# Optimization experiments

Measured on AMD Instinct MI355X. Metric: run time of the kernel, lower is better.

The kernel has to match this reference:

```python
import jax, jax.numpy as jnp
import numpy as np
import math

HEAD_DIM = 64
RP_DIM = 256
B, H, N = 4, 8, 4096
EPS = 1e-4  # performer positive-feature epsilon


def _ortho_gaussian_matrix(m, d, seed=0):
    # gaussian_orthogonal_random_matrix, scaling=0: stack QR-orthogonalized
    # d x d gaussian blocks, scale rows by norms of an iid gaussian matrix.
    rng = np.random.default_rng(seed)
    blocks = []
    for _ in range(int(np.ceil(m / d))):
        g = rng.standard_normal((d, d))
        q, _ = np.linalg.qr(g)
        blocks.append(q.T)
    mat = np.concatenate(blocks, axis=0)[:m]
    multiplier = np.linalg.norm(rng.standard_normal((m, d)), axis=1)
    return (multiplier[:, None] * mat).astype(np.float32)


def _softmax_features(x, proj, is_query):
    # FAVOR+ positive random features: ratio * exp(Wx - ||x||^2/2 - stab) + eps
    ratio = proj.shape[0] ** -0.5
    xp = jnp.einsum('bhnd,md->bhnm', x, proj)
    diag = 0.5 * jnp.sum(x * x, axis=-1, keepdims=True)
    if is_query:
        stab = jnp.max(xp, axis=-1, keepdims=True)
    else:
        stab = jnp.max(xp, axis=(-1, -2), keepdims=True)
    return ratio * (jnp.exp(xp - diag - stab) + EPS)


def setup_inputs() -> dict:
    key = jax.random.key(0)
    kq, kk, kv = jax.random.split(key, 3)
    Q = jax.random.normal(kq, (B, H, N, HEAD_DIM), dtype=jnp.float32)
    K = jax.random.normal(kk, (B, H, N, HEAD_DIM), dtype=jnp.float32)
    V = jax.random.normal(kv, (B, H, N, HEAD_DIM), dtype=jnp.float32)
    mask = jnp.ones((B, N), dtype=jnp.float32)
    projection = jnp.asarray(_ortho_gaussian_matrix(RP_DIM, HEAD_DIM, seed=0))
    return {'Q': Q, 'K': K, 'V': V, 'mask': mask, 'projection': projection}


def reference(Q, K, V, mask, projection):
    scale = HEAD_DIM ** -0.25  # 1/sqrt(sqrt(head_dim))
    m = mask[:, None, :, None]
    q = Q * scale
    k = K * scale * m
    v = V * m
    phi_q = _softmax_features(q, projection, is_query=True)   # [b,h,n,m]
    phi_k = _softmax_features(k, projection, is_query=False)  # [b,h,n,m]
    # non-causal linear attention
    k_sum = jnp.sum(phi_k, axis=2)                                   # [b,h,m]
    D_inv = 1.0 / jnp.einsum('bhnm,bhm->bhn', phi_q, k_sum)          # [b,h,n]
    context = jnp.einsum('bhnm,bhne->bhme', phi_k, v)                # [b,h,m,e]
    out = jnp.einsum('bhme,bhnm,bhn->bhne', context, phi_q, D_inv)   # [b,h,n,e]
    return out
```

## Files before the change

kernel.cpp:

```cpp
#include <hip/hip_runtime.h>
#include <hip/hip_bf16.h>


typedef __attribute__((ext_vector_type(8))) short short8;
typedef __attribute__((ext_vector_type(4))) float floatx4;

constexpr int BB = 4, HH = 8, NN = 4096, DD = 64, MM = 256, BH = 32;
constexpr int NCH = 16;
constexpr float SCALE = 0.3535533905932738f;
constexpr float RATIO = 0.0625f;
constexpr float EPSI  = 1e-4f;
constexpr float NEGINF = -3.4e38f;

__device__ inline unsigned pk2(float a, float b) {
  unsigned ua = __float_as_uint(a) + 0x8000u;
  unsigned ub = __float_as_uint(b) + 0x8000u;
  return (ua >> 16) | (ub & 0xffff0000u);
}
__device__ inline float hif(float x) {
  return __uint_as_float((__float_as_uint(x) + 0x8000u) & 0xffff0000u);
}
__device__ inline unsigned short bhi(float x) {
  return (unsigned short)((__float_as_uint(x) + 0x8000u) >> 16);
}
__device__ inline int ph16(int i) { return (i & 56) | ((i + (i >> 3)) & 7); }

union Frag { short8 s8; unsigned u[4]; };

__device__ inline void atomicMaxF(float* a, float v) {
  unsigned* ai = (unsigned*)a;
  unsigned old = __atomic_load_n(ai, __ATOMIC_RELAXED);
  while (__uint_as_float(old) < v) {
    unsigned assumed = old;
    old = atomicCAS(ai, assumed, __float_as_uint(v));
    if (old == assumed) break;
  }
}

__global__ __launch_bounds__(256) void prep_kernel(
    const float* __restrict__ proj, unsigned short* __restrict__ projH,
    unsigned short* __restrict__ projL, float* __restrict__ stabk,
    float* __restrict__ Vs, float* __restrict__ ctxsum,
    float* __restrict__ ksE) {
  const int i = blockIdx.x * 256 + threadIdx.x;
  float v = proj[i];
  projH[i] = bhi(v);
  projL[i] = bhi(v - hif(v));
  if (i < BH) stabk[i] = NEGINF;
  if (i < 2048) { Vs[i] = 0.f; ctxsum[i] = 0.f; }
  if (i < 8192) ksE[i] = 0.f;
}

template <bool PARTIAL>
__global__ __launch_bounds__(256) void kside_kernel(
    const float* __restrict__ K, const float* __restrict__ V,
    const float* __restrict__ mask,
    const unsigned short* __restrict__ projH, const unsigned short* __restrict__ projL,
    float* __restrict__ stabk, float* __restrict__ ksE,
    float* __restrict__ ctxOut, float* __restrict__ Vs) {
  const int bh = blockIdx.y, b = bh >> 3;
  const int t = threadIdx.x;
  const int w = t >> 6, l = t & 63, c = l & 15, sq = l >> 4;
  const int m0 = w * 64;

  __shared__ __align__(16) unsigned short sK[2][32 * 72];
  __shared__ __align__(16) unsigned short sVt[2][64 * 40];
  __shared__ float sDiag[32];
  __shared__ float sRed[4];
  __shared__ float sVsum[4][64];
  __shared__ __align__(16) unsigned short sPhi[4][2][512];

  Frag Bp[4][2][2];
#pragma unroll
  for (int tt = 0; tt < 4; ++tt)
#pragma unroll
    for (int s = 0; s < 2; ++s) {
      const size_t o = (size_t)(m0 + tt * 16 + c) * DD + s * 32 + sq * 8;
      Bp[tt][s][0].s8 = *(const short8*)&projH[o];
      Bp[tt][s][1].s8 = *(const short8*)&projL[o];
    }

  floatx4 ctxacc[4][4];
#pragma unroll
  for (int i = 0; i < 4; ++i)
#pragma unroll
    for (int j = 0; j < 4; ++j) ctxacc[i][j] = (floatx4){0.f, 0.f, 0.f, 0.f};
  float ksac[4] = {0.f, 0.f, 0.f, 0.f};
  float mxloc = NEGINF;
  float vsacc = 0.f;

  const int r0 = blockIdx.x * 256;

  for (int ch = 0; ch < 8; ++ch) {
    const int rb = r0 + ch * 32;
    __syncthreads();

#pragma unroll
    for (int rep = 0; rep < 2; ++rep) {
      const int f = t + rep * 256;
      const int n = f >> 4, dg = f & 15;
      const float mk = mask[b * NN + rb + n];
      const float msc = mk * SCALE;
      float4 kv = *(const float4*)(K + ((size_t)bh * NN + rb + n) * DD + dg * 4);
      float k0 = kv.x * msc, k1 = kv.y * msc, k2 = kv.z * msc, k3 = kv.w * msc;
      float ss = fmaf(k0, k0, fmaf(k1, k1, fmaf(k2, k2, k3 * k3)));
      ss += __shfl_xor(ss, 1); ss += __shfl_xor(ss, 2);
      ss += __shfl_xor(ss, 4); ss += __shfl_xor(ss, 8);
      if (dg == 0) sDiag[n] = 0.5f * ss;
      unsigned h0 = pk2(k0, k1), h1 = pk2(k2, k3);
      float q0 = k0 - hif(k0), q1 = k1 - hif(k1);
      float q2 = k2 - hif(k2), q3 = k3 - hif(k3);
      *(uint2*)(&sK[0][n * 72 + dg * 4]) = make_uint2(h0, h1);
      *(uint2*)(&sK[1][n * 72 + dg * 4]) = make_uint2(pk2(q0, q1), pk2(q2, q3));
    }

#pragma unroll
    for (int rep = 0; rep < 2; ++rep) {
      const int nb = w * 4 + rep * 16;
      const int n_loc = nb + sq;
      const float mk = mask[b * NN + rb + n_loc];
      float4 vv = *(const float4*)(V + ((size_t)bh * NN + rb + n_loc) * DD + c * 4);
      float va[4] = {vv.x * mk, vv.y * mk, vv.z * mk, vv.w * mk};
      float g[4];
#pragma unroll
      for (int k = 0; k < 4; ++k) {
        const int gi = (sq + k) & 3;
        float sel = va[(sq - k) & 3];
        g[gi] = __shfl(sel, gi * 16 + c);
      }
      const int estar = c * 4 + sq;
      vsacc += ((g[0] + g[1]) + (g[2] + g[3]));
      unsigned h0 = pk2(g[0], g[1]), h1 = pk2(g[2], g[3]);
      float q0 = g[0] - hif(g[0]), q1 = g[1] - hif(g[1]);
      float q2 = g[2] - hif(g[2]), q3 = g[3] - hif(g[3]);
      *(uint2*)(&sVt[0][estar * 40 + nb]) = make_uint2(h0, h1);
      *(uint2*)(&sVt[1][estar * 40 + nb]) = make_uint2(pk2(q0, q1), pk2(q2, q3));
    }
    __syncthreads();

    Frag Ak[2][2][2];
#pragma unroll
    for (int i = 0; i < 2; ++i)
#pragma unroll
      for (int s = 0; s < 2; ++s) {
        Ak[i][s][0].s8 = *(const short8*)&sK[0][(i * 16 + c) * 72 + s * 32 + sq * 8];
        Ak[i][s][1].s8 = *(const short8*)&sK[1][(i * 16 + c) * 72 + s * 32 + sq * 8];
      }
    Frag Bv[4][2];
#pragma unroll
    for (int E = 0; E < 4; ++E) {
      Bv[E][0].s8 = *(const short8*)&sVt[0][(E * 16 + c) * 40 + sq * 8];
      Bv[E][1].s8 = *(const short8*)&sVt[1][(E * 16 + c) * 40 + sq * 8];
    }

#pragma unroll
    for (int tt = 0; tt < 4; ++tt) {
      floatx4 xacc[2];
#pragma unroll
      for (int i = 0; i < 2; ++i) {
        floatx4 a = (floatx4){0.f, 0.f, 0.f, 0.f};
#pragma unroll
        for (int s = 0; s < 2; ++s) {
          a = __builtin_amdgcn_mfma_f32_16x16x32_bf16(Ak[i][s][0].s8, Bp[tt][s][0].s8, a, 0, 0, 0);
          a = __builtin_amdgcn_mfma_f32_16x16x32_bf16(Ak[i][s][0].s8, Bp[tt][s][1].s8, a, 0, 0, 0);
          a = __builtin_amdgcn_mfma_f32_16x16x32_bf16(Ak[i][s][1].s8, Bp[tt][s][0].s8, a, 0, 0, 0);
        }
        xacc[i] = a;
      }
      const int qp_c = sq >> 1, half = (sq & 1) * 4;
#pragma unroll
      for (int i = 0; i < 2; ++i) {
        float p[4];
#pragma unroll
        for (int jj = 0; jj < 4; ++jj) {
          float xp = xacc[i][jj];
          mxloc = fmaxf(mxloc, xp);
          p[jj] = __expf(xp - sDiag[i * 16 + sq * 4 + jj]);
          ksac[tt] += p[jj];
        }
        unsigned h0 = pk2(p[0], p[1]), h1 = pk2(p[2], p[3]);
        float q0 = p[0] - hif(p[0]), q1 = p[1] - hif(p[1]);
        float q2 = p[2] - hif(p[2]), q3 = p[3] - hif(p[3]);
        const int tl = (i * 2 + qp_c) * 16 + c;
        const int idx = ph16(tl) * 8 + half;
        *(uint2*)&sPhi[w][0][idx] = make_uint2(h0, h1);
        *(uint2*)&sPhi[w][1][idx] = make_uint2(pk2(q0, q1), pk2(q2, q3));
      }
      Frag Ap[2];
      Ap[0].s8 = *(const short8*)&sPhi[w][0][ph16(l) * 8];
      Ap[1].s8 = *(const short8*)&sPhi[w][1][ph16(l) * 8];
#pragma unroll
      for (int E = 0; E < 4; ++E) {
        ctxacc[tt][E] = __builtin_amdgcn_mfma_f32_16x16x32_bf16(Ap[0].s8, Bv[E][0].s8, ctxacc[tt][E], 0, 0, 0);
        ctxacc[tt][E] = __builtin_amdgcn_mfma_f32_16x16x32_bf16(Ap[0].s8, Bv[E][1].s8, ctxacc[tt][E], 0, 0, 0);
        ctxacc[tt][E] = __builtin_amdgcn_mfma_f32_16x16x32_bf16(Ap[1].s8, Bv[E][0].s8, ctxacc[tt][E], 0, 0, 0);
      }
    }
  }

#pragma unroll
  for (int tt = 0; tt < 4; ++tt) {
    float v = ksac[tt];
    v += __shfl_xor(v, 16);
    v += __shfl_xor(v, 32);
    if (sq == 0) atomicAdd(&ksE[bh * MM + m0 + tt * 16 + c], v);
  }
#pragma unroll
  for (int off = 1; off <= 32; off <<= 1) mxloc = fmaxf(mxloc, __shfl_xor(mxloc, off));
  if (l == 0) sRed[w] = mxloc;
  sVsum[w][c * 4 + sq] = vsacc;
  __syncthreads();
  if (t == 0)
    atomicMaxF(&stabk[bh], fmaxf(fmaxf(sRed[0], sRed[1]), fmaxf(sRed[2], sRed[3])));
  if (t < 64)
    atomicAdd(&Vs[bh * DD + t],
              (sVsum[0][t] + sVsum[1][t]) + (sVsum[2][t] + sVsum[3][t]));

  if (PARTIAL) {
    float* cg = ctxOut + ((size_t)(bh * NCH + blockIdx.x) * MM) * DD;
#pragma unroll
    for (int tt = 0; tt < 4; ++tt)
#pragma unroll
      for (int E = 0; E < 4; ++E)
#pragma unroll
        for (int r = 0; r < 4; ++r)
          cg[(m0 + tt * 16 + sq * 4 + r) * DD + E * 16 + c] = ctxacc[tt][E][r];
  } else {
    float* cg = ctxOut + (size_t)bh * MM * DD;
#pragma unroll
    for (int tt = 0; tt < 4; ++tt)
#pragma unroll
      for (int E = 0; E < 4; ++E)
#pragma unroll
        for (int r = 0; r < 4; ++r)
          atomicAdd(&cg[(m0 + tt * 16 + sq * 4 + r) * DD + E * 16 + c],
                    ctxacc[tt][E][r]);
  }
}

template <int NPARTS>
__global__ __launch_bounds__(256) void fixup_kernel(
    const float* __restrict__ stabk, const float* __restrict__ Vs,
    const float* __restrict__ ksE, const float* __restrict__ ctxParts,
    float* __restrict__ ksum, float* __restrict__ kssum,
    float* __restrict__ ctxsum, unsigned short* __restrict__ ctxTH,
    unsigned short* __restrict__ ctxTL) {
  const int bh = blockIdx.y, mc = blockIdx.x, t = threadIdx.x;
  const float es = __expf(-stabk[bh]);
  const int e = t & 63, g = t >> 6;
  const float vse = EPSI * Vs[bh * DD + e];

  __shared__ float tile[64 * 33];
  __shared__ float cred[256];

  float csum = 0.f;
#pragma unroll
  for (int r = 0; r < 8; ++r) {
    const int ml = r * 4 + g;
    const int m = mc * 32 + ml;
    float x = 0.f;
#pragma unroll
    for (int p = 0; p < NPARTS; ++p)
      x += ctxParts[(((size_t)bh * NPARTS + p) * MM + m) * DD + e];
    float v = RATIO * (es * x + vse);
    csum += v;
    tile[e * 33 + ml] = v;
  }
  cred[t] = csum;
  __syncthreads();
  if (t < 64)
    atomicAdd(&ctxsum[bh * DD + t],
              (cred[t] + cred[t + 64]) + (cred[t + 128] + cred[t + 192]));

  {
    const int ml5 = t & 31, elg = t >> 5;
#pragma unroll
    for (int r = 0; r < 8; ++r) {
      const int el = r * 8 + elg;
      float v = tile[el * 33 + ml5];
      const size_t o = ((size_t)(bh * DD + el)) * MM + mc * 32 + ml5;
      ctxTH[o] = bhi(v);
      ctxTL[o] = bhi(v - hif(v));
    }
  }

  if (mc == 0) {
    __syncthreads();
    const float kv = RATIO * (es * ksE[bh * MM + t] + (float)NN * EPSI);
    ksum[bh * MM + t] = kv;
    cred[t] = kv;
    __syncthreads();
    for (int off = 128; off >= 1; off >>= 1) {
      if (t < off) cred[t] += cred[t + off];
      __syncthreads();
    }
    if (t == 0) kssum[bh] = cred[0];
  }
}

__global__ __launch_bounds__(256, 2) void out_kernel(
    const float* __restrict__ Q,
    const unsigned short* __restrict__ projH, const unsigned short* __restrict__ projL,
    const float* __restrict__ ksum,
    const unsigned short* __restrict__ ctxTH, const unsigned short* __restrict__ ctxTL,
    const float* __restrict__ kssum, const float* __restrict__ ctxsum,
    float* __restrict__ out) {
  const int bh = blockIdx.y;
  const int r0 = blockIdx.x * 64;
  const int t = threadIdx.x, w = t >> 6, l = t & 63, c = l & 15, sq = l >> 4;

  __shared__ __align__(16) unsigned short sQ[2][64 * 80];
  __shared__ __align__(16) unsigned short sP[2][64 * 80];
  __shared__ __align__(16) unsigned short sC[2][64 * 80];
  __shared__ float sKs[256];
  __shared__ float sDiag[64];
  __shared__ __align__(16) unsigned short sPhi[4][2][2][512];

  {
    const int row = t >> 2, q4 = t & 3;
    const float* qp = Q + ((size_t)bh * NN + r0 + row) * DD + q4 * 16;
    float4 t0 = *(const float4*)(qp + 0), t1 = *(const float4*)(qp + 4),
           t2 = *(const float4*)(qp + 8), t3 = *(const float4*)(qp + 12);
    float v[16] = {t0.x, t0.y, t0.z, t0.w, t1.x, t1.y, t1.z, t1.w,
                   t2.x, t2.y, t2.z, t2.w, t3.x, t3.y, t3.z, t3.w};
    float ss = 0.f;
#pragma unroll
    for (int j = 0; j < 16; ++j) { v[j] *= SCALE; ss = fmaf(v[j], v[j], ss); }
    ss += __shfl_xor(ss, 1);
    ss += __shfl_xor(ss, 2);
    if (q4 == 0) sDiag[row] = 0.5f * ss;
    unsigned short* dh = &sQ[0][row * 80 + q4 * 16];
    unsigned short* dl = &sQ[1][row * 80 + q4 * 16];
#pragma unroll
    for (int j = 0; j < 8; ++j) {
      *(unsigned*)&dh[2 * j] = pk2(v[2 * j], v[2 * j + 1]);
      float l0 = v[2 * j] - hif(v[2 * j]), l1 = v[2 * j + 1] - hif(v[2 * j + 1]);
      *(unsigned*)&dl[2 * j] = pk2(l0, l1);
    }
  }
  sKs[t] = ksum[bh * MM + t];
  __syncthreads();

  Frag Bq[2][2];
#pragma unroll
  for (int s = 0; s < 2; ++s)
#pragma unroll
    for (int p = 0; p < 2; ++p)
      Bq[s][p].s8 = *(const short8*)&sQ[p][(w * 16 + c) * 80 + s * 32 + sq * 8];

  const float diagc = sDiag[w * 16 + c];
  floatx4 oacc[4];
#pragma unroll
  for (int E = 0; E < 4; ++E) oacc[E] = (floatx4){0.f, 0.f, 0.f, 0.f};
  float mxacc = NEGINF, dsacc = 0.f;

  for (int mc = 0; mc < 4; ++mc) {
    __syncthreads();
    {
      const int row = t >> 2, q4 = t & 3;
      const size_t gp = (size_t)(mc * 64 + row) * DD + q4 * 16;
      const uint4* ph = (const uint4*)&projH[gp];
      const uint4* pl = (const uint4*)&projL[gp];
      *(uint4*)&sP[0][row * 80 + q4 * 16] = ph[0];
      *(uint4*)&sP[0][row * 80 + q4 * 16 + 8] = ph[1];
      *(uint4*)&sP[1][row * 80 + q4 * 16] = pl[0];
      *(uint4*)&sP[1][row * 80 + q4 * 16 + 8] = pl[1];
      const size_t gc = ((size_t)bh * DD + row) * MM + mc * 64 + q4 * 16;
      const uint4* chh = (const uint4*)&ctxTH[gc];
      const uint4* cll = (const uint4*)&ctxTL[gc];
      *(uint4*)&sC[0][row * 80 + q4 * 16] = chh[0];
      *(uint4*)&sC[0][row * 80 + q4 * 16 + 8] = chh[1];
      *(uint4*)&sC[1][row * 80 + q4 * 16] = cll[0];
      *(uint4*)&sC[1][row * 80 + q4 * 16 + 8] = cll[1];
    }
    __syncthreads();

#pragma unroll
    for (int tt = 0; tt < 4; ++tt) {
      Frag Af[2][2];
#pragma unroll
      for (int s = 0; s < 2; ++s)
#pragma unroll
        for (int p = 0; p < 2; ++p)
          Af[s][p].s8 = *(const short8*)&sP[p][(tt * 16 + c) * 80 + s * 32 + sq * 8];
      floatx4 x = (floatx4){0.f, 0.f, 0.f, 0.f};
#pragma unroll
      for (int s = 0; s < 2; ++s) {
        x = __builtin_amdgcn_mfma_f32_16x16x32_bf16(Af[s][0].s8, Bq[s][0].s8, x, 0, 0, 0);
        x = __builtin_amdgcn_mfma_f32_16x16x32_bf16(Af[s][0].s8, Bq[s][1].s8, x, 0, 0, 0);
        x = __builtin_amdgcn_mfma_f32_16x16x32_bf16(Af[s][1].s8, Bq[s][0].s8, x, 0, 0, 0);
      }
      float p4[4];
#pragma unroll
      for (int jj = 0; jj < 4; ++jj) {
        const float xp = x[jj];
        mxacc = fmaxf(mxacc, xp);
        p4[jj] = __expf(xp - diagc);
        dsacc = fmaf(p4[jj], sKs[mc * 64 + tt * 16 + sq * 4 + jj], dsacc);
      }
      const int kstep = tt >> 1;
      const int tl = ((tt & 1) * 2 + (sq >> 1)) * 16 + c;
      const int off = (sq & 1) * 4;
      float l0 = p4[0] - hif(p4[0]), l1 = p4[1] - hif(p4[1]);
      float l2 = p4[2] - hif(p4[2]), l3 = p4[3] - hif(p4[3]);
      *(uint2*)&sPhi[w][0][kstep][tl * 8 + off] = make_uint2(pk2(p4[0], p4[1]), pk2(p4[2], p4[3]));
      *(uint2*)&sPhi[w][1][kstep][tl * 8 + off] = make_uint2(pk2(l0, l1), pk2(l2, l3));
    }

#pragma unroll
    for (int ks = 0; ks < 2; ++ks) {
      Frag Aph[2];
      Aph[0].s8 = *(const short8*)&sPhi[w][0][ks][l * 8];
      Aph[1].s8 = *(const short8*)&sPhi[w][1][ks][l * 8];
#pragma unroll
      for (int E = 0; E < 4; ++E) {
        Frag Bc0, Bc1;
        Bc0.s8 = *(const short8*)&sC[0][(E * 16 + c) * 80 + ks * 32 + sq * 8];
        Bc1.s8 = *(const short8*)&sC[1][(E * 16 + c) * 80 + ks * 32 + sq * 8];
        oacc[E] = __builtin_amdgcn_mfma_f32_16x16x32_bf16(Aph[0].s8, Bc0.s8, oacc[E], 0, 0, 0);
        oacc[E] = __builtin_amdgcn_mfma_f32_16x16x32_bf16(Aph[0].s8, Bc1.s8, oacc[E], 0, 0, 0);
        oacc[E] = __builtin_amdgcn_mfma_f32_16x16x32_bf16(Aph[1].s8, Bc0.s8, oacc[E], 0, 0, 0);
      }
    }
  }

  mxacc = fmaxf(mxacc, __shfl_xor(mxacc, 16));
  mxacc = fmaxf(mxacc, __shfl_xor(mxacc, 32));
  dsacc += __shfl_xor(dsacc, 16);
  dsacc += __shfl_xor(dsacc, 32);

  const float kss = kssum[bh];
  float fac[4], oinv[4];
#pragma unroll
  for (int jj = 0; jj < 4; ++jj) {
    const int src = sq * 4 + jj;
    const float s_row = __shfl(mxacc, src);
    const float d_row = __shfl(dsacc, src);
    const float f = __expf(s_row) * EPSI;
    fac[jj] = f;
    oinv[jj] = 1.f / (d_row + f * kss);
  }

  const float* csb = ctxsum + bh * DD;
#pragma unroll
  for (int E = 0; E < 4; ++E) {
    const float cse = csb[E * 16 + c];
#pragma unroll
    for (int jj = 0; jj < 4; ++jj) {
      const int row = r0 + w * 16 + sq * 4 + jj;
      out[((size_t)bh * NN + row) * DD + E * 16 + c] =
          (oacc[E][jj] + fac[jj] * cse) * oinv[jj];
    }
  }
}

extern "C" void kernel_launch(void* const* d_in, const int* in_sizes, int n_in,
                              void* d_out, int out_size, void* d_ws, size_t ws_size,
                              hipStream_t stream) {
  const float* Q    = (const float*)d_in[0];
  const float* K    = (const float*)d_in[1];
  const float* V    = (const float*)d_in[2];
  const float* mask = (const float*)d_in[3];
  const float* proj = (const float*)d_in[4];
  float* out = (float*)d_out;

  float* wsf = (float*)d_ws;
  float* stabk  = wsf;
  float* ksum   = wsf + 32;
  float* kssum  = wsf + 8224;
  float* Vs     = wsf + 8256;
  float* ctxsum = wsf + 10304;
  float* ksE    = wsf + 12352;
  unsigned short* projH = (unsigned short*)(wsf + 20544);
  unsigned short* projL = (unsigned short*)(wsf + 28736);
  unsigned short* ctxTH = (unsigned short*)(wsf + 36928);
  unsigned short* ctxTL = (unsigned short*)(wsf + 299072);
  float* ctxBig = wsf + 561216;

  const size_t need_partial = (size_t)(561216 + NCH * BH * MM * DD) * 4;
  const bool partial = ws_size >= need_partial;

  prep_kernel<<<64, 256, 0, stream>>>(proj, projH, projL, stabk, Vs, ctxsum, ksE);

  if (partial) {
    kside_kernel<true><<<dim3(NCH, BH), 256, 0, stream>>>(
        K, V, mask, projH, projL, stabk, ksE, ctxBig, Vs);
    fixup_kernel<NCH><<<dim3(8, BH), 256, 0, stream>>>(
        stabk, Vs, ksE, ctxBig, ksum, kssum, ctxsum, ctxTH, ctxTL);
  } else {
    hipMemsetAsync(ctxBig, 0, (size_t)MM * DD * BH * 4, stream);
    kside_kernel<false><<<dim3(NCH, BH), 256, 0, stream>>>(
        K, V, mask, projH, projL, stabk, ksE, ctxBig, Vs);
    fixup_kernel<1><<<dim3(8, BH), 256, 0, stream>>>(
        stabk, Vs, ksE, ctxBig, ksum, kssum, ctxsum, ctxTH, ctxTL);
  }

  out_kernel<<<dim3(64, BH), 256, 0, stream>>>(
      Q, projH, projL, ksum, ctxTH, ctxTL, kssum, ctxsum, out);
}
```

Before: 255.2 us.

## Split kside feature dimension across two blocks and prefetch next K/V chunk

The K-side kernel grid is doubled so each block handles half of the 256 random features (128 per block, 32 per wave), halving per-thread accumulators and projection fragments. It adds launch_bounds occupancy hints and software-prefetches the next chunk's K, V and mask into registers while the current chunk's MFMAs run. This trades duplicated K/V loads and K-side conversion work across the two feature halves for higher parallelism, occupancy and latency hiding. The V-sum atomic is restricted to one half to avoid double counting.

Measured after the change: 451.9 us. 1.77x slower.

```diff
diff --git a/kernel.cpp b/kernel.cpp
--- a/kernel.cpp
+++ b/kernel.cpp
@@ -52,16 +52,18 @@
 }
 
 template <bool PARTIAL>
-__global__ __launch_bounds__(256) void kside_kernel(
+__global__ __launch_bounds__(256, 4) void kside_kernel(
     const float* __restrict__ K, const float* __restrict__ V,
     const float* __restrict__ mask,
     const unsigned short* __restrict__ projH, const unsigned short* __restrict__ projL,
     float* __restrict__ stabk, float* __restrict__ ksE,
     float* __restrict__ ctxOut, float* __restrict__ Vs) {
   const int bh = blockIdx.y, b = bh >> 3;
+  const int nch = blockIdx.x & (NCH - 1);
+  const int ms  = blockIdx.x >> 4;
   const int t = threadIdx.x;
   const int w = t >> 6, l = t & 63, c = l & 15, sq = l >> 4;
-  const int m0 = w * 64;
+  const int m0 = ms * 128 + w * 32;
 
   __shared__ __align__(16) unsigned short sK[2][32 * 72];
   __shared__ __align__(16) unsigned short sVt[2][64 * 40];
@@ -70,9 +72,9 @@
   __shared__ float sVsum[4][64];
   __shared__ __align__(16) unsigned short sPhi[4][2][512];
 
-  Frag Bp[4][2][2];
-#pragma unroll
-  for (int tt = 0; tt < 4; ++tt)
+  Frag Bp[2][2][2];
+#pragma unroll
+  for (int tt = 0; tt < 2; ++tt)
 #pragma unroll
     for (int s = 0; s < 2; ++s) {
       const size_t o = (size_t)(m0 + tt * 16 + c) * DD + s * 32 + sq * 8;
@@ -80,29 +82,43 @@
       Bp[tt][s][1].s8 = *(const short8*)&projL[o];
     }
 
-  floatx4 ctxacc[4][4];
-#pragma unroll
-  for (int i = 0; i < 4; ++i)
+  floatx4 ctxacc[2][4];
+#pragma unroll
+  for (int i = 0; i < 2; ++i)
 #pragma unroll
     for (int j = 0; j < 4; ++j) ctxacc[i][j] = (floatx4){0.f, 0.f, 0.f, 0.f};
-  float ksac[4] = {0.f, 0.f, 0.f, 0.f};
+  float ksac[2] = {0.f, 0.f};
   float mxloc = NEGINF;
   float vsacc = 0.f;
 
-  const int r0 = blockIdx.x * 256;
+  const int r0 = nch * 256;
+
+  float4 pk4[2], pv4[2];
+  float pmk[2], pmv[2];
+  {
+    const int rb = r0;
+#pragma unroll
+    for (int rep = 0; rep < 2; ++rep) {
+      const int f = t + rep * 256;
+      const int n = f >> 4;
+      pmk[rep] = mask[b * NN + rb + n];
+      pk4[rep] = *(const float4*)(K + ((size_t)bh * NN + rb + n) * DD + (f & 15) * 4);
+      const int n_loc = w * 4 + rep * 16 + sq;
+      pmv[rep] = mask[b * NN + rb + n_loc];
+      pv4[rep] = *(const float4*)(V + ((size_t)bh * NN + rb + n_loc) * DD + c * 4);
+    }
+  }
 
   for (int ch = 0; ch < 8; ++ch) {
-    const int rb = r0 + ch * 32;
     __syncthreads();
 
 #pragma unroll
     for (int rep = 0; rep < 2; ++rep) {
       const int f = t + rep * 256;
       const int n = f >> 4, dg = f & 15;
-      const float mk = mask[b * NN + rb + n];
-      const float msc = mk * SCALE;
-      float4 kv = *(const float4*)(K + ((size_t)bh * NN + rb + n) * DD + dg * 4);
-      float k0 = kv.x * msc, k1 = kv.y * msc, k2 = kv.z * msc, k3 = kv.w * msc;
+      const float msc = pmk[rep] * SCALE;
+      float k0 = pk4[rep].x * msc, k1 = pk4[rep].y * msc,
+            k2 = pk4[rep].z * msc, k3 = pk4[rep].w * msc;
       float ss = fmaf(k0, k0, fmaf(k1, k1, fmaf(k2, k2, k3 * k3)));
       ss += __shfl_xor(ss, 1); ss += __shfl_xor(ss, 2);
       ss += __shfl_xor(ss, 4); ss += __shfl_xor(ss, 8);
@@ -117,9 +133,8 @@
 #pragma unroll
     for (int rep = 0; rep < 2; ++rep) {
       const int nb = w * 4 + rep * 16;
-      const int n_loc = nb + sq;
-      const float mk = mask[b * NN + rb + n_loc];
-      float4 vv = *(const float4*)(V + ((size_t)bh * NN + rb + n_loc) * DD + c * 4);
+      const float mk = pmv[rep];
+      float4 vv = pv4[rep];
       float va[4] = {vv.x * mk, vv.y * mk, vv.z * mk, vv.w * mk};
       float g[4];
 #pragma unroll
@@ -153,8 +168,22 @@
       Bv[E][1].s8 = *(const short8*)&sVt[1][(E * 16 + c) * 40 + sq * 8];
     }
 
-#pragma unroll
-    for (int tt = 0; tt < 4; ++tt) {
+    if (ch < 7) {
+      const int rb = r0 + (ch + 1) * 32;
+#pragma unroll
+      for (int rep = 0; rep < 2; ++rep) {
+        const int f = t + rep * 256;
+        const int n = f >> 4;
+        pmk[rep] = mask[b * NN + rb + n];
+        pk4[rep] = *(const float4*)(K + ((size_t)bh * NN + rb + n) * DD + (f & 15) * 4);
+        const int n_loc = w * 4 + rep * 16 + sq;
+        pmv[rep] = mask[b * NN + rb + n_loc];
+        pv4[rep] = *(const float4*)(V + ((size_t)bh * NN + rb + n_loc) * DD + c * 4);
+      }
+    }
+
+#pragma unroll
+    for (int tt = 0; tt < 2; ++tt) {
       floatx4 xacc[2];
 #pragma unroll
       for (int i = 0; i < 2; ++i) {
@@ -199,7 +228,7 @@
   }
 
 #pragma unroll
-  for (int tt = 0; tt < 4; ++tt) {
+  for (int tt = 0; tt < 2; ++tt) {
     float v = ksac[tt];
     v += __shfl_xor(v, 16);
     v += __shfl_xor(v, 32);
@@ -212,14 +241,14 @@
   __syncthreads();
   if (t == 0)
     atomicMaxF(&stabk[bh], fmaxf(fmaxf(sRed[0], sRed[1]), fmaxf(sRed[2], sRed[3])));
-  if (t < 64)
+  if (ms == 0 && t < 64)
     atomicAdd(&Vs[bh * DD + t],
               (sVsum[0][t] + sVsum[1][t]) + (sVsum[2][t] + sVsum[3][t]));
 
   if (PARTIAL) {
-    float* cg = ctxOut + ((size_t)(bh * NCH + blockIdx.x) * MM) * DD;
-#pragma unroll
-    for (int tt = 0; tt < 4; ++tt)
+    float* cg = ctxOut + ((size_t)(bh * NCH + nch) * MM) * DD;
+#pragma unroll
+    for (int tt = 0; tt < 2; ++tt)
 #pragma unroll
       for (int E = 0; E < 4; ++E)
 #pragma unroll
@@ -228,7 +257,7 @@
   } else {
     float* cg = ctxOut + (size_t)bh * MM * DD;
 #pragma unroll
-    for (int tt = 0; tt < 4; ++tt)
+    for (int tt = 0; tt < 2; ++tt)
 #pragma unroll
       for (int E = 0; E < 4; ++E)
 #pragma unroll
@@ -483,13 +512,13 @@
   prep_kernel<<<64, 256, 0, stream>>>(proj, projH, projL, stabk, Vs, ctxsum, ksE);
 
   if (partial) {
-    kside_kernel<true><<<dim3(NCH, BH), 256, 0, stream>>>(
+    kside_kernel<true><<<dim3(NCH * 2, BH), 256, 0, stream>>>(
         K, V, mask, projH, projL, stabk, ksE, ctxBig, Vs);
     fixup_kernel<NCH><<<dim3(8, BH), 256, 0, stream>>>(
         stabk, Vs, ksE, ctxBig, ksum, kssum, ctxsum, ctxTH, ctxTL);
   } else {
     hipMemsetAsync(ctxBig, 0, (size_t)MM * DD * BH * 4, stream);
-    kside_kernel<false><<<dim3(NCH, BH), 256, 0, stream>>>(
+    kside_kernel<false><<<dim3(NCH * 2, BH), 256, 0, stream>>>(
         K, V, mask, projH, projL, stabk, ksE, ctxBig, Vs);
     fixup_kernel<1><<<dim3(8, BH), 256, 0, stream>>>(
         stabk, Vs, ksE, ctxBig, ksum, kssum, ctxsum, ctxTH, ctxTL);
```
